# Kernel tuning notes

Measured on AMD Instinct MI355X. Metric: run time of the kernel, lower is better.

## Reference

```python
import jax, jax.numpy as jnp
import numpy as np

D_MODEL = 1024
NUM_HEADS = 16
HEAD_DIM = D_MODEL // NUM_HEADS


def setup_inputs() -> dict:
    key = jax.random.key(0)
    ks = jax.random.split(key, 5)
    s = 0.02
    x = jax.random.normal(ks[0], (4, 2048, D_MODEL), dtype=jnp.float32)
    W_Q = jax.random.normal(ks[1], (D_MODEL, D_MODEL), dtype=jnp.float32) * s
    W_K = jax.random.normal(ks[2], (D_MODEL, D_MODEL), dtype=jnp.float32) * s
    W_V = jax.random.normal(ks[3], (D_MODEL, D_MODEL), dtype=jnp.float32) * s
    W_O = jax.random.normal(ks[4], (D_MODEL, D_MODEL), dtype=jnp.float32) * s
    return {"x": x, "W_Q": W_Q, "W_K": W_K, "W_V": W_V, "W_O": W_O}


def reference(x, W_Q, W_K, W_V, W_O):
    b, s, d = x.shape
    h, hd = NUM_HEADS, HEAD_DIM
    scale = 1.0 / np.sqrt(hd).astype(np.float32)
    # nn.Linear applies x @ W.T; split heads then transpose -> (b, h, s, hd)
    def split(W):
        return (x @ W.T).reshape(b, s, h, hd).transpose(0, 2, 1, 3)
    Q, K, V = split(W_Q), split(W_K), split(W_V)
    scores = jnp.einsum('bhqd,bhkd->bhqk', Q, K) * scale
    causal = jnp.triu(jnp.ones((s, s), dtype=bool), k=1)
    scores = jnp.where(causal, -jnp.inf, scores)
    weights = jax.nn.softmax(scores, axis=-1)
    ctx = jnp.einsum('bhqk,bhkd->bhqd', weights, V)
    ctx = ctx.transpose(0, 2, 1, 3).reshape(b, s, d)
    return ctx @ W_O.T
```

## Files before the change

### kernel.cpp

```cpp
#include <hip/hip_runtime.h>


#define B_  4
#define S_  2048
#define D_  1024
#define H_  16
#define HD_ 64

typedef __attribute__((ext_vector_type(8))) short bf16x8;
typedef __attribute__((ext_vector_type(4))) float f32x4;

#define MFMA16 __builtin_amdgcn_mfma_f32_16x16x32_bf16

__device__ __forceinline__ unsigned short f2b(float f) {
  unsigned u = __builtin_bit_cast(unsigned, f);
  unsigned r = (u + 0x7FFFu + ((u >> 16) & 1u)) >> 16;
  return (unsigned short)r;
}

__device__ __forceinline__ unsigned cvtpk(float lo, float hi) {
  unsigned r;
  asm("v_cvt_pk_bf16_f32 %0, %1, %2" : "=v"(r) : "v"(lo), "v"(hi));
  return r;
}

__device__ __forceinline__ void gll16(const void* g, const void* l) {
  __builtin_amdgcn_global_load_lds(
      (const __attribute__((address_space(1))) unsigned int*)g,
      (__attribute__((address_space(3))) unsigned int*)l, 16, 0, 0);
}

__global__ __launch_bounds__(256) void cvt_all(
    const float4* __restrict__ x,  const float4* __restrict__ wq,
    const float4* __restrict__ wk, const float4* __restrict__ wv,
    const float4* __restrict__ wo,
    ushort4* __restrict__ xb,  ushort4* __restrict__ wqb,
    ushort4* __restrict__ wkb, ushort4* __restrict__ wvb,
    ushort4* __restrict__ wob)
{
  const int y = blockIdx.y;
  const float4* in; ushort4* out;
  if (y < 8)       { in = x  + (size_t)y * 262144; out = xb  + (size_t)y * 262144; }
  else if (y == 8) { in = wq; out = wqb; }
  else if (y == 9) { in = wk; out = wkb; }
  else if (y == 10){ in = wv; out = wvb; }
  else             { in = wo; out = wob; }
  int i = blockIdx.x * 256 + threadIdx.x;
  float4 v = in[i];
  ushort4 o;
  o.x = f2b(v.x); o.y = f2b(v.y); o.z = f2b(v.z); o.w = f2b(v.w);
  out[i] = o;
}

#define GSTG(BF, K0) { \
    _Pragma("unroll") for (int t = 0; t < 2; ++t) { \
      const int grow_ = t*64 + w*16 + srow; \
      const int lbas_ = (t*256 + w*64) * 8; \
      gll16(A  + (size_t)(arow + grow_)*1024 + (K0) + scol, &As[BF][lbas_]); \
      gll16(Bw + (size_t)(brow + grow_)*1024 + (K0) + scol, &Bs[BF][lbas_]); } }

#define GSTEP(BF, SW) { \
    bf16x8 af[4], bfr[4]; \
    _Pragma("unroll") for (int i = 0; i < 4; ++i) \
      af[i]  = *(const bf16x8*)(&As[BF][(wm*64 + i*16 + r16)*32 + g*8]); \
    _Pragma("unroll") for (int i = 0; i < 4; ++i) \
      bfr[i] = *(const bf16x8*)(&Bs[BF][(wn*64 + i*16 + r16)*32 + g*8]); \
    _Pragma("unroll") for (int i = 0; i < 4; ++i) \
      _Pragma("unroll") for (int j = 0; j < 4; ++j) \
        acc[i][j] = (SW) ? MFMA16(bfr[j], af[i], acc[i][j], 0, 0, 0) \
                         : MFMA16(af[i], bfr[j], acc[i][j], 0, 0, 0); }

template<int MODE>
__global__ __launch_bounds__(256) void gemm_bt(
    const unsigned short* __restrict__ A,
    const unsigned short* __restrict__ B0,
    const unsigned short* __restrict__ B1,
    unsigned short* __restrict__ O0,
    unsigned short* __restrict__ O1,
    float* __restrict__ OF)
{
  const int tid  = threadIdx.x;
  const int lane = tid & 63;
  const int w    = tid >> 6;
  const int wm   = w >> 1, wn = w & 1;
  const int r16  = lane & 15, g = lane >> 4;

  const int orig = blockIdx.x + 64 * blockIdx.y;
  const int t_   = orig >> 3;
  const int bm   = (orig & 7) * 8 + (t_ & 7);
  const int bn   = t_ >> 3;

  const unsigned short* Bw = (MODE == 0 && blockIdx.z == 1) ? B1 : B0;
  unsigned short* Ob       = (MODE == 0 && blockIdx.z == 1) ? O1 : O0;

  __shared__ unsigned short As[2][4096];
  __shared__ unsigned short Bs[2][4096];

  const int arow = bm * 128, brow = bn * 128;
  const int srow = lane >> 2, scol = (lane & 3) * 8;
  constexpr bool SW = (MODE == 2);

  f32x4 acc[4][4] = {};
  GSTG(0, 0);
  for (int kt = 0; kt < 32; kt += 2) {
    __syncthreads();
    GSTG(1, (kt + 1) * 32);
    GSTEP(0, SW);
    __syncthreads();
    if (kt + 2 < 32) GSTG(0, (kt + 2) * 32);
    GSTEP(1, SW);
  }

  #pragma unroll
  for (int i = 0; i < 4; ++i) {
    #pragma unroll
    for (int j = 0; j < 4; ++j) {
      #pragma unroll
      for (int r = 0; r < 4; ++r) {
        float v = acc[i][j][r];
        if (MODE == 1) {
          int m = arow + wm*64 + i*16 + g*4 + r;
          int n = brow + wn*64 + j*16 + r16;
          OF[(size_t)m * 1024 + n] = v;
        } else if (MODE == 0) {
          int m = arow + wm*64 + i*16 + g*4 + r;
          int n = brow + wn*64 + j*16 + r16;
          float scl = (blockIdx.z == 0) ? 0.18033688f : 1.0f;
          int b = m >> 11, s = m & 2047, h = n >> 6, hd = n & 63;
          Ob[((((size_t)b*H_ + h)*S_) + s)*HD_ + hd] = f2b(v * scl);
        } else {
          int n = brow + wn*64 + j*16 + g*4 + r;
          int m = arow + wm*64 + i*16 + r16;
          int b = m >> 11, s = m & 2047, h = n >> 6, hd = n & 63;
          O0[(((size_t)b*H_ + h)*HD_ + hd)*S_ + s] = f2b(v);
        }
      }
    }
  }
}

#define ASTG(BF, KB) { \
    gll16(Kh + (size_t)((KB) + tr0 +     rsub)*HD_ + csw, &KVb[BF][0][ tr0     *64]); \
    gll16(Kh + (size_t)((KB) + tr0 + 8 + rsub)*HD_ + csw, &KVb[BF][0][(tr0 + 8)*64]); \
    gll16(Vh + (size_t)(tr0 +     rsub)*S_ + (KB) + csw,  &KVb[BF][1][ tr0     *64]); \
    gll16(Vh + (size_t)(tr0 + 8 + rsub)*S_ + (KB) + csw,  &KVb[BF][1][(tr0 + 8)*64]); }

#define ACOMP(BF, KB) { \
    const int kb_ = (KB); \
    if (kb_ <= qw) { \
      f32x4 sc[4]; \
      __builtin_amdgcn_s_setprio(1); \
      _Pragma("unroll") for (int c = 0; c < 4; ++c) { \
        bf16x8 kf0 = *(const bf16x8*)((const char*)&KVb[BF][0][0] + (c*16 + r16)*128 + ((( g      ^ (r16 & 7)) & 7) << 4)); \
        bf16x8 kf1 = *(const bf16x8*)((const char*)&KVb[BF][0][0] + (c*16 + r16)*128 + ((((4 + g) ^ (r16 & 7)) & 7) << 4)); \
        f32x4 s_ = {}; \
        s_ = MFMA16(kf0, qf[0], s_, 0, 0, 0); \
        s_ = MFMA16(kf1, qf[1], s_, 0, 0, 0); \
        sc[c] = s_; } \
      __builtin_amdgcn_s_setprio(0); \
      f32x4 p4[4]; \
      if (kb_ + 63 > qw) { \
        const int qrow_ = qw + r16; \
        _Pragma("unroll") for (int c = 0; c < 4; ++c) \
          _Pragma("unroll") for (int r = 0; r < 4; ++r) \
            p4[c][r] = (kb_ + c*16 + g*4 + r > qrow_) ? 0.f : exp2f(sc[c][r]); \
      } else { \
        _Pragma("unroll") for (int c = 0; c < 4; ++c) \
          _Pragma("unroll") for (int r = 0; r < 4; ++r) \
            p4[c][r] = exp2f(sc[c][r]); } \
      { char* prp_ = Plw + r16*128; \
        const int swz_ = (r16 & 7) << 4; \
        _Pragma("unroll") for (int c = 0; c < 4; ++c) { \
          uint2 pw_; \
          pw_.x = cvtpk(p4[c][0], p4[c][1]); \
          pw_.y = cvtpk(p4[c][2], p4[c][3]); \
          *(uint2*)(prp_ + ((c*32 + g*8) ^ swz_)) = pw_; } } \
      __builtin_amdgcn_s_setprio(1); \
      _Pragma("unroll") for (int kc = 0; kc < 2; ++kc) { \
        bf16x8 pf_ = *(const bf16x8*)(Plw + r16*128 + ((kc*64 + g*16) ^ ((r16 & 7) << 4))); \
        oL = MFMA16(onesf, pf_, oL, 0, 0, 0); \
        _Pragma("unroll") for (int dn = 0; dn < 4; ++dn) { \
          bf16x8 vf_ = *(const bf16x8*)((const char*)&KVb[BF][1][0] + (dn*16 + r16)*128 + ((((kc*4 + g) ^ (r16 & 7)) & 7) << 4)); \
          oT[dn] = MFMA16(vf_, pf_, oT[dn], 0, 0, 0); } } \
      __builtin_amdgcn_s_setprio(0); \
    } }

__global__ __launch_bounds__(256, 4) void attn_fwd(
    const unsigned short* __restrict__ Q,
    const unsigned short* __restrict__ K,
    const unsigned short* __restrict__ Vt,
    unsigned short* __restrict__ C)
{
  const int tid  = threadIdx.x;
  const int lane = tid & 63;
  const int w    = tid >> 6;
  const int r16  = lane & 15, g = lane >> 4;

  const int l_   = blockIdx.x;
  const int bh   = (l_ & 7) * 8 + ((l_ >> 3) & 7);
  const int px   = l_ >> 6;
  const int bb   = bh >> 4, hh = bh & 15;

  const unsigned short* Qh = Q  + (size_t)bh * S_ * HD_;
  const unsigned short* Kh = K  + (size_t)bh * S_ * HD_;
  const unsigned short* Vh = Vt + (size_t)bh * HD_ * S_;

  __shared__ unsigned short KVb[2][2][4096];
  __shared__ unsigned short Pl[4][1024];
  char* Plw = (char*)&Pl[w][0];

  const int rsub = lane >> 3;
  const int csw  = ((lane & 7) ^ rsub) * 8;
  const int tr0  = w * 16;

  bf16x8 onesf;
  #pragma unroll
  for (int j = 0; j < 8; ++j) onesf[j] = (short)0x3F80;

  ASTG(0, 0);

  #pragma unroll
  for (int ph = 0; ph < 2; ++ph) {
    const int jt = ph ? (31 - px) : px;
    const int q0 = jt * 64;
    const int qw = q0 + w * 16;
    const int nt = (jt + 2) & ~1;

    bf16x8 qf[2];
    #pragma unroll
    for (int dh = 0; dh < 2; ++dh)
      qf[dh] = *(const bf16x8*)(&Qh[(size_t)(qw + r16) * HD_ + dh*32 + g*8]);

    f32x4 oT[4] = {};
    f32x4 oL = {};

    for (int kt = 0; kt < nt; kt += 2) {
      __syncthreads();
      ASTG(1, (kt + 1) * 64);
      ACOMP(0, kt * 64);
      __syncthreads();
      if (kt + 2 < nt)      { ASTG(0, (kt + 2) * 64); }
      else if (ph == 0)     { ASTG(0, 0); }
      ACOMP(1, (kt + 1) * 64);
    }

    float inv = 1.0f / oL[0];
    int tok = bb * S_ + qw + r16;
    #pragma unroll
    for (int dn = 0; dn < 4; ++dn) {
      uint2 cw;
      cw.x = cvtpk(oT[dn][0] * inv, oT[dn][1] * inv);
      cw.y = cvtpk(oT[dn][2] * inv, oT[dn][3] * inv);
      *(uint2*)(&C[(size_t)tok * D_ + hh*HD_ + dn*16 + g*4]) = cw;
    }
  }
}

extern "C" void kernel_launch(void* const* d_in, const int* in_sizes, int n_in,
                              void* d_out, int out_size, void* d_ws, size_t ws_size,
                              hipStream_t stream) {
  const float* x  = (const float*)d_in[0];
  const float* Wq = (const float*)d_in[1];
  const float* Wk = (const float*)d_in[2];
  const float* Wv = (const float*)d_in[3];
  const float* Wo = (const float*)d_in[4];

  char* ws = (char*)d_ws;
  unsigned short* xb  = (unsigned short*)(ws);
  unsigned short* Wqb = (unsigned short*)(ws + 16777216);
  unsigned short* Wkb = (unsigned short*)(ws + 18874368);
  unsigned short* Wvb = (unsigned short*)(ws + 20971520);
  unsigned short* Wob = (unsigned short*)(ws + 23068672);
  unsigned short* Qb  = (unsigned short*)(ws + 25165824);
  unsigned short* Kb  = (unsigned short*)(ws + 41943040);
  unsigned short* Vtb = (unsigned short*)(ws + 58720256);
  unsigned short* Cb  = (unsigned short*)(ws + 75497472);

  cvt_all<<<dim3(1024, 12), 256, 0, stream>>>(
      (const float4*)x, (const float4*)Wq, (const float4*)Wk,
      (const float4*)Wv, (const float4*)Wo,
      (ushort4*)xb, (ushort4*)Wqb, (ushort4*)Wkb, (ushort4*)Wvb, (ushort4*)Wob);

  gemm_bt<0><<<dim3(64, 8, 2), 256, 0, stream>>>(xb, Wqb, Wkb, Qb, Kb, nullptr);
  gemm_bt<2><<<dim3(64, 8, 1), 256, 0, stream>>>(xb, Wvb, nullptr, Vtb, nullptr, nullptr);
  attn_fwd<<<1024, 256, 0, stream>>>(Qb, Kb, Vtb, Cb);
  gemm_bt<1><<<dim3(64, 8, 1), 256, 0, stream>>>(Cb, Wob, nullptr, nullptr, nullptr, (float*)d_out);
}
```

Baseline: 186.6 us.

## Fuse QKV projections into one GEMM launch and restructure causal attention scheduling

The Q, K and V projections now run as a single GEMM launch over the contiguous bf16 weight buffer. Each block picks its Q/K or transposed-V epilogue from its column tile. Operand order is swapped per mode so epilogues write packed 4-element vector stores instead of scalar stores. The attention kernel drops the paired short/long query tiles per block and launches one query tile per block, heaviest first, with a single K buffer, a double-buffered V buffer and an occupancy hint raised from 4 to 5. This removes one launch and the scalar store traffic, at the cost of relying on hardware scheduling rather than explicit pairing to balance the causal workload.

```diff
diff --git a/kernel.cpp b/kernel.cpp
--- a/kernel.cpp
+++ b/kernel.cpp
@@ -56,8 +56,8 @@
     _Pragma("unroll") for (int t = 0; t < 2; ++t) { \
       const int grow_ = t*64 + w*16 + srow; \
       const int lbas_ = (t*256 + w*64) * 8; \
-      gll16(A  + (size_t)(arow + grow_)*1024 + (K0) + scol, &As[BF][lbas_]); \
-      gll16(Bw + (size_t)(brow + grow_)*1024 + (K0) + scol, &Bs[BF][lbas_]); } }
+      gll16(A + (size_t)(arow + grow_)*1024 + (K0) + scol, &As[BF][lbas_]); \
+      gll16(W + (size_t)(brow + grow_)*1024 + (K0) + scol, &Bs[BF][lbas_]); } }
 
 #define GSTEP(BF, SW) { \
     bf16x8 af[4], bfr[4]; \
@@ -70,13 +70,23 @@
         acc[i][j] = (SW) ? MFMA16(bfr[j], af[i], acc[i][j], 0, 0, 0) \
                          : MFMA16(af[i], bfr[j], acc[i][j], 0, 0, 0); }
 
+#define GLOOP(SW) \
+  for (int kt = 0; kt < 32; kt += 2) { \
+    __syncthreads(); \
+    GSTG(1, (kt + 1) * 32); \
+    GSTEP(0, SW); \
+    __syncthreads(); \
+    if (kt + 2 < 32) GSTG(0, (kt + 2) * 32); \
+    GSTEP(1, SW); \
+  }
+
 template<int MODE>
 __global__ __launch_bounds__(256) void gemm_bt(
     const unsigned short* __restrict__ A,
-    const unsigned short* __restrict__ B0,
-    const unsigned short* __restrict__ B1,
-    unsigned short* __restrict__ O0,
-    unsigned short* __restrict__ O1,
+    const unsigned short* __restrict__ W,
+    unsigned short* __restrict__ OQ,
+    unsigned short* __restrict__ OK,
+    unsigned short* __restrict__ OV,
     float* __restrict__ OF)
 {
   const int tid  = threadIdx.x;
@@ -90,74 +100,87 @@
   const int bm   = (orig & 7) * 8 + (t_ & 7);
   const int bn   = t_ >> 3;
 
-  const unsigned short* Bw = (MODE == 0 && blockIdx.z == 1) ? B1 : B0;
-  unsigned short* Ob       = (MODE == 0 && blockIdx.z == 1) ? O1 : O0;
-
   __shared__ unsigned short As[2][4096];
   __shared__ unsigned short Bs[2][4096];
 
   const int arow = bm * 128, brow = bn * 128;
   const int srow = lane >> 2, scol = (lane & 3) * 8;
-  constexpr bool SW = (MODE == 2);
 
   f32x4 acc[4][4] = {};
+  const bool vblk = (MODE == 0) && (bn >= 16);
   GSTG(0, 0);
-  for (int kt = 0; kt < 32; kt += 2) {
-    __syncthreads();
-    GSTG(1, (kt + 1) * 32);
-    GSTEP(0, SW);
-    __syncthreads();
-    if (kt + 2 < 32) GSTG(0, (kt + 2) * 32);
-    GSTEP(1, SW);
+  if (!vblk) { GLOOP(true) } else { GLOOP(false) }
+
+  if (MODE == 1) {
+    #pragma unroll
+    for (int i = 0; i < 4; ++i)
+      #pragma unroll
+      for (int j = 0; j < 4; ++j) {
+        int t = arow + wm*64 + i*16 + r16;
+        int f = brow + wn*64 + j*16 + g*4;
+        float4 st;
+        st.x = acc[i][j][0]; st.y = acc[i][j][1];
+        st.z = acc[i][j][2]; st.w = acc[i][j][3];
+        *(float4*)(&OF[(size_t)t * 1024 + f]) = st;
+      }
+  } else if (!vblk) {
+    unsigned short* Od = (bn < 8) ? OQ : OK;
+    const float scl = (bn < 8) ? 0.18033688f : 1.0f;
+    #pragma unroll
+    for (int i = 0; i < 4; ++i)
+      #pragma unroll
+      for (int j = 0; j < 4; ++j) {
+        int t = arow + wm*64 + i*16 + r16;
+        int f = (brow & 1023) + wn*64 + j*16 + g*4;
+        int b = t >> 11, s = t & 2047, h = f >> 6, hd = f & 63;
+        uint2 cw;
+        cw.x = cvtpk(acc[i][j][0] * scl, acc[i][j][1] * scl);
+        cw.y = cvtpk(acc[i][j][2] * scl, acc[i][j][3] * scl);
+        *(uint2*)(&Od[((((size_t)b*H_ + h)*S_) + s)*HD_ + hd]) = cw;
+      }
+  } else {
+    #pragma unroll
+    for (int i = 0; i < 4; ++i)
+      #pragma unroll
+      for (int j = 0; j < 4; ++j) {
+        int t0 = arow + wm*64 + i*16 + g*4;
+        int f  = (brow & 1023) + wn*64 + j*16 + r16;
+        int b = t0 >> 11, s = t0 & 2047, h = f >> 6, hd = f & 63;
+        uint2 cw;
+        cw.x = cvtpk(acc[i][j][0], acc[i][j][1]);
+        cw.y = cvtpk(acc[i][j][2], acc[i][j][3]);
+        *(uint2*)(&OV[(((size_t)b*H_ + h)*HD_ + hd)*S_ + s]) = cw;
+      }
   }
-
-  #pragma unroll
-  for (int i = 0; i < 4; ++i) {
-    #pragma unroll
-    for (int j = 0; j < 4; ++j) {
-      #pragma unroll
-      for (int r = 0; r < 4; ++r) {
-        float v = acc[i][j][r];
-        if (MODE == 1) {
-          int m = arow + wm*64 + i*16 + g*4 + r;
-          int n = brow + wn*64 + j*16 + r16;
-          OF[(size_t)m * 1024 + n] = v;
-        } else if (MODE == 0) {
-          int m = arow + wm*64 + i*16 + g*4 + r;
-          int n = brow + wn*64 + j*16 + r16;
-          float scl = (blockIdx.z == 0) ? 0.18033688f : 1.0f;
-          int b = m >> 11, s = m & 2047, h = n >> 6, hd = n & 63;
-          Ob[((((size_t)b*H_ + h)*S_) + s)*HD_ + hd] = f2b(v * scl);
-        } else {
-          int n = brow + wn*64 + j*16 + g*4 + r;
-          int m = arow + wm*64 + i*16 + r16;
-          int b = m >> 11, s = m & 2047, h = n >> 6, hd = n & 63;
-          O0[(((size_t)b*H_ + h)*HD_ + hd)*S_ + s] = f2b(v);
-        }
-      }
-    }
-  }
-}
-
-#define ASTG(BF, KB) { \
-    gll16(Kh + (size_t)((KB) + tr0 +     rsub)*HD_ + csw, &KVb[BF][0][ tr0     *64]); \
-    gll16(Kh + (size_t)((KB) + tr0 + 8 + rsub)*HD_ + csw, &KVb[BF][0][(tr0 + 8)*64]); \
-    gll16(Vh + (size_t)(tr0 +     rsub)*S_ + (KB) + csw,  &KVb[BF][1][ tr0     *64]); \
-    gll16(Vh + (size_t)(tr0 + 8 + rsub)*S_ + (KB) + csw,  &KVb[BF][1][(tr0 + 8)*64]); }
-
-#define ACOMP(BF, KB) { \
+}
+
+#define ASTG_K(KB) { \
+    gll16(Kh + (size_t)((KB) + tr0 +     rsub)*HD_ + csw, &Ks[ tr0     *64]); \
+    gll16(Kh + (size_t)((KB) + tr0 + 8 + rsub)*HD_ + csw, &Ks[(tr0 + 8)*64]); }
+
+#define ASTG_V(VP, KB) { \
+    gll16(Vh + (size_t)(tr0 +     rsub)*S_ + (KB) + csw, &Vs[VP][ tr0     *64]); \
+    gll16(Vh + (size_t)(tr0 + 8 + rsub)*S_ + (KB) + csw, &Vs[VP][(tr0 + 8)*64]); }
+
+#define ATILE(VP, KB) { \
     const int kb_ = (KB); \
-    if (kb_ <= qw) { \
-      f32x4 sc[4]; \
+    const bool act_ = (kb_ <= qw); \
+    __syncthreads();                        \
+    f32x4 sc[4]; \
+    if (act_) { \
       __builtin_amdgcn_s_setprio(1); \
       _Pragma("unroll") for (int c = 0; c < 4; ++c) { \
-        bf16x8 kf0 = *(const bf16x8*)((const char*)&KVb[BF][0][0] + (c*16 + r16)*128 + ((( g      ^ (r16 & 7)) & 7) << 4)); \
-        bf16x8 kf1 = *(const bf16x8*)((const char*)&KVb[BF][0][0] + (c*16 + r16)*128 + ((((4 + g) ^ (r16 & 7)) & 7) << 4)); \
+        bf16x8 kf0 = *(const bf16x8*)((const char*)&Ks[0] + (c*16 + r16)*128 + ((( g      ^ (r16 & 7)) & 7) << 4)); \
+        bf16x8 kf1 = *(const bf16x8*)((const char*)&Ks[0] + (c*16 + r16)*128 + ((((4 + g) ^ (r16 & 7)) & 7) << 4)); \
         f32x4 s_ = {}; \
         s_ = MFMA16(kf0, qf[0], s_, 0, 0, 0); \
         s_ = MFMA16(kf1, qf[1], s_, 0, 0, 0); \
         sc[c] = s_; } \
       __builtin_amdgcn_s_setprio(0); \
+    } \
+    __syncthreads();                        \
+    if (kb_ + 64 < lim) { ASTG_K(kb_ + 64); ASTG_V(VP ^ 1, kb_ + 64); } \
+    if (act_) { \
       f32x4 p4[4]; \
       if (kb_ + 63 > qw) { \
         const int qrow_ = qw + r16; \
@@ -180,12 +203,12 @@
         bf16x8 pf_ = *(const bf16x8*)(Plw + r16*128 + ((kc*64 + g*16) ^ ((r16 & 7) << 4))); \
         oL = MFMA16(onesf, pf_, oL, 0, 0, 0); \
         _Pragma("unroll") for (int dn = 0; dn < 4; ++dn) { \
-          bf16x8 vf_ = *(const bf16x8*)((const char*)&KVb[BF][1][0] + (dn*16 + r16)*128 + ((((kc*4 + g) ^ (r16 & 7)) & 7) << 4)); \
+          bf16x8 vf_ = *(const bf16x8*)((const char*)&Vs[VP][0] + (dn*16 + r16)*128 + ((((kc*4 + g) ^ (r16 & 7)) & 7) << 4)); \
           oT[dn] = MFMA16(vf_, pf_, oT[dn], 0, 0, 0); } } \
       __builtin_amdgcn_s_setprio(0); \
     } }
 
-__global__ __launch_bounds__(256, 4) void attn_fwd(
+__global__ __launch_bounds__(256, 5) void attn_fwd(
     const unsigned short* __restrict__ Q,
     const unsigned short* __restrict__ K,
     const unsigned short* __restrict__ Vt,
@@ -198,14 +221,15 @@
 
   const int l_   = blockIdx.x;
   const int bh   = (l_ & 7) * 8 + ((l_ >> 3) & 7);
-  const int px   = l_ >> 6;
+  const int jt   = 31 - (l_ >> 6);
   const int bb   = bh >> 4, hh = bh & 15;
 
   const unsigned short* Qh = Q  + (size_t)bh * S_ * HD_;
   const unsigned short* Kh = K  + (size_t)bh * S_ * HD_;
   const unsigned short* Vh = Vt + (size_t)bh * HD_ * S_;
 
-  __shared__ unsigned short KVb[2][2][4096];
+  __shared__ unsigned short Ks[4096];
+  __shared__ unsigned short Vs[2][4096];
   __shared__ unsigned short Pl[4][1024];
   char* Plw = (char*)&Pl[w][0];
 
@@ -217,42 +241,36 @@
   #pragma unroll
   for (int j = 0; j < 8; ++j) onesf[j] = (short)0x3F80;
 
-  ASTG(0, 0);
-
+  const int q0  = jt * 64;
+  const int qw  = q0 + w * 16;
+  const int nt  = jt + 1;
+  const int nte = (nt + 1) & ~1;
+  const int lim = nte * 64;
+
+  bf16x8 qf[2];
   #pragma unroll
-  for (int ph = 0; ph < 2; ++ph) {
-    const int jt = ph ? (31 - px) : px;
-    const int q0 = jt * 64;
-    const int qw = q0 + w * 16;
-    const int nt = (jt + 2) & ~1;
-
-    bf16x8 qf[2];
-    #pragma unroll
-    for (int dh = 0; dh < 2; ++dh)
-      qf[dh] = *(const bf16x8*)(&Qh[(size_t)(qw + r16) * HD_ + dh*32 + g*8]);
-
-    f32x4 oT[4] = {};
-    f32x4 oL = {};
-
-    for (int kt = 0; kt < nt; kt += 2) {
-      __syncthreads();
-      ASTG(1, (kt + 1) * 64);
-      ACOMP(0, kt * 64);
-      __syncthreads();
-      if (kt + 2 < nt)      { ASTG(0, (kt + 2) * 64); }
-      else if (ph == 0)     { ASTG(0, 0); }
-      ACOMP(1, (kt + 1) * 64);
-    }
-
-    float inv = 1.0f / oL[0];
-    int tok = bb * S_ + qw + r16;
-    #pragma unroll
-    for (int dn = 0; dn < 4; ++dn) {
-      uint2 cw;
-      cw.x = cvtpk(oT[dn][0] * inv, oT[dn][1] * inv);
-      cw.y = cvtpk(oT[dn][2] * inv, oT[dn][3] * inv);
-      *(uint2*)(&C[(size_t)tok * D_ + hh*HD_ + dn*16 + g*4]) = cw;
-    }
+  for (int dh = 0; dh < 2; ++dh)
+    qf[dh] = *(const bf16x8*)(&Qh[(size_t)(qw + r16) * HD_ + dh*32 + g*8]);
+
+  f32x4 oT[4] = {};
+  f32x4 oL = {};
+
+  ASTG_K(0);
+  ASTG_V(0, 0);
+
+  for (int kt = 0; kt < nte; kt += 2) {
+    ATILE(0, kt * 64);
+    ATILE(1, kt * 64 + 64);
+  }
+
+  float inv = 1.0f / oL[0];
+  int tok = bb * S_ + qw + r16;
+  #pragma unroll
+  for (int dn = 0; dn < 4; ++dn) {
+    uint2 cw;
+    cw.x = cvtpk(oT[dn][0] * inv, oT[dn][1] * inv);
+    cw.y = cvtpk(oT[dn][2] * inv, oT[dn][3] * inv);
+    *(uint2*)(&C[(size_t)tok * D_ + hh*HD_ + dn*16 + g*4]) = cw;
   }
 }
 
@@ -281,8 +299,8 @@
       (const float4*)Wv, (const float4*)Wo,
       (ushort4*)xb, (ushort4*)Wqb, (ushort4*)Wkb, (ushort4*)Wvb, (ushort4*)Wob);
 
-  gemm_bt<0><<<dim3(64, 8, 2), 256, 0, stream>>>(xb, Wqb, Wkb, Qb, Kb, nullptr);
-  gemm_bt<2><<<dim3(64, 8, 1), 256, 0, stream>>>(xb, Wvb, nullptr, Vtb, nullptr, nullptr);
-  attn_fwd<<<1024, 256, 0, stream>>>(Qb, Kb, Vtb, Cb);
-  gemm_bt<1><<<dim3(64, 8, 1), 256, 0, stream>>>(Cb, Wob, nullptr, nullptr, nullptr, (float*)d_out);
-}
+  gemm_bt<0><<<dim3(64, 24), 256, 0, stream>>>(xb, Wqb, Qb, Kb, Vtb, nullptr);
+  attn_fwd<<<2048, 256, 0, stream>>>(Qb, Kb, Vtb, Cb);
+  gemm_bt<1><<<dim3(64, 8), 256, 0, stream>>>(Cb, Wob, nullptr, nullptr, nullptr,
+                                              (float*)d_out);
+}
```

Measured after the change: 228.1 us. 1.22x slower.
